# Kernel tuning notes

Measured on AMD Instinct MI355X. Metric: run time of the kernel, lower is better.

Reference implementation:

```python
import jax, jax.numpy as jnp
import numpy as np

H, W = 32, 56
CK, CV = 64, 512
N = 16 * H * W  # long + work memory fully populated: 16 frames of H*W entries
TOP_K = 30


def setup_inputs() -> dict:
    key = jax.random.key(0)
    k1, k2, k3, k4, k5 = jax.random.split(key, 5)
    return {
        "q_key": jax.random.normal(k1, (1, CK, H, W), dtype=jnp.float32),
        "q_selection": jax.random.uniform(k2, (1, CK, H, W), dtype=jnp.float32),
        "mem_key": jax.random.normal(k3, (1, CK, N), dtype=jnp.float32),
        "mem_shrinkage": jax.random.uniform(k4, (1, N, 1), dtype=jnp.float32),
        "mem_value": jax.random.normal(k5, (2, CV, N), dtype=jnp.float32),
    }


def reference(q_key, q_selection, mem_key, mem_shrinkage, mem_value):
    b, ck, h, w = q_key.shape
    hw = h * w
    qk = q_key.reshape(1, ck, hw)          # [1, CK, HW]
    qs = q_selection.reshape(1, ck, hw)    # [1, CK, HW]

    mk = jnp.swapaxes(mem_key, 1, 2)       # [1, N, CK]
    # negative weighted squared L2 distance via matmul algebra
    a_sq = jnp.matmul(mk * mk, qs)                    # [1, N, HW]
    two_ab = 2.0 * jnp.matmul(mk, qk * qs)            # [1, N, HW]
    b_sq = jnp.sum(qs * qk * qk, axis=1, keepdims=True)  # [1, 1, HW]
    sim = (-a_sq + two_ab - b_sq) * mem_shrinkage / jnp.sqrt(jnp.float32(ck))  # [1, N, HW]

    # topk over the memory axis (dim=1), softmax over selected entries, scatter back
    simT = jnp.swapaxes(sim, 1, 2)                    # [1, HW, N]
    vals, idx = jax.lax.top_k(simT, TOP_K)            # [1, HW, K]
    x_exp = jnp.exp(vals)
    x_exp = x_exp / jnp.sum(x_exp, axis=-1, keepdims=True)
    i0 = jnp.arange(1)[:, None, None]
    i1 = jnp.arange(hw)[None, :, None]
    affT = jnp.zeros_like(simT).at[i0, i1, idx].set(x_exp)  # [1, HW, N]
    affinity = jnp.swapaxes(affT, 1, 2)               # [1, N, HW]

    out = jnp.matmul(mem_value, affinity)             # [2, CV, HW] (batch-broadcast)
    return out.reshape(2, CV, h, w)
```

## Files before the change

### kernel.cpp

```cpp
#include <hip/hip_runtime.h>
#include <math.h>

#define HW      1792
#define NMEM    28672
#define NCHUNK  3584
#define TOPK    30
#define KSEL    48
#define SCAP    64
#define SIMB    448
#define WPS     7

typedef __attribute__((ext_vector_type(8))) short bf16x8;
typedef __attribute__((ext_vector_type(8))) unsigned short u16x8;
typedef __attribute__((ext_vector_type(4))) float f32x4;
typedef __attribute__((ext_vector_type(4))) _Float16 h4;
typedef unsigned long long ull;

static __device__ __forceinline__ unsigned short f2bf(float v) {
  unsigned b = __float_as_uint(v);
  return (unsigned short)((b + 0x7FFFu + ((b >> 16) & 1u)) >> 16);
}
static __device__ __forceinline__ float bf2f(unsigned short h) {
  return __uint_as_float(((unsigned)h) << 16);
}
static __device__ __forceinline__ unsigned fkey(float v) {
  return __float_as_uint(-v) & 0x7FFFFFFFu;
}
static __device__ __forceinline__ ull umax64(ull a, ull b) { return a > b ? a : b; }
static __device__ __forceinline__ ull umin64(ull a, ull b) { return a < b ? a : b; }
static __device__ __forceinline__ void gl_lds16(const void* g, void* l) {
  __builtin_amdgcn_global_load_lds(
      (const __attribute__((address_space(1))) unsigned*)g,
      (__attribute__((address_space(3))) unsigned*)l, 16, 0, 0);
}
#define WSYNC() do { asm volatile("s_waitcnt lgkmcnt(0)" ::: "memory"); \
                     __builtin_amdgcn_wave_barrier(); } while (0)

__global__ __launch_bounds__(256)
void k_prep_b(const float* __restrict__ mk, const float* __restrict__ shr_in,
              unsigned short* __restrict__ Bh,
              float* __restrict__ mkT, float* __restrict__ shr_s)
{
  const int n = blockIdx.x * 256 + threadIdx.x;
  shr_s[n] = shr_in[n] * 0.125f;
  for (int cb = 0; cb < 64; cb += 8) {
    u16x8 h1, h2;
    float vv[8];
    #pragma unroll
    for (int j = 0; j < 8; ++j) {
      float v = mk[(size_t)(cb + j) * NMEM + n];
      vv[j] = v;
      h1[j] = f2bf(v);
      h2[j] = f2bf(v * v);
    }
    const int s = cb >> 3;
    *reinterpret_cast<u16x8*>(&Bh[((size_t)s * NMEM + n) * 8])       = h1;
    *reinterpret_cast<u16x8*>(&Bh[((size_t)(s + 8) * NMEM + n) * 8]) = h2;
    *reinterpret_cast<float4*>(&mkT[(size_t)n * 64 + cb])     = make_float4(vv[0], vv[1], vv[2], vv[3]);
    *reinterpret_cast<float4*>(&mkT[(size_t)n * 64 + cb + 4]) = make_float4(vv[4], vv[5], vv[6], vv[7]);
  }
}

__global__ __launch_bounds__(256)
void k_prep_u(const float* __restrict__ q_key, const float* __restrict__ q_sel,
              unsigned short* __restrict__ Uh, unsigned short* __restrict__ Ul,
              float* __restrict__ bsq)
{
  const int p = blockIdx.x * 256 + threadIdx.x;
  float bs = 0.f;
  for (int cb = 0; cb < 64; cb += 8) {
    u16x8 h1, l1, h2, l2;
    #pragma unroll
    for (int j = 0; j < 8; ++j) {
      int c = cb + j;
      float k = q_key[(size_t)c * HW + p];
      float s = q_sel[(size_t)c * HW + p];
      float u = 2.f * k * s;
      float w = -s;
      bs = fmaf(s * k, k, bs);
      unsigned short h = f2bf(u); h1[j] = h; l1[j] = f2bf(u - bf2f(h));
      unsigned short g = f2bf(w); h2[j] = g; l2[j] = f2bf(w - bf2f(g));
    }
    const int s = cb >> 3;
    *reinterpret_cast<u16x8*>(&Uh[((size_t)s * HW + p) * 8])       = h1;
    *reinterpret_cast<u16x8*>(&Ul[((size_t)s * HW + p) * 8])       = l1;
    *reinterpret_cast<u16x8*>(&Uh[((size_t)(s + 8) * HW + p) * 8]) = h2;
    *reinterpret_cast<u16x8*>(&Ul[((size_t)(s + 8) * HW + p) * 8]) = l2;
  }
  bsq[p] = bs;
}

__global__ __launch_bounds__(256, 2)
void k_sim(const unsigned short* __restrict__ Uh, const unsigned short* __restrict__ Ul,
           const unsigned short* __restrict__ Bh,
           const float* __restrict__ bsq, const float* __restrict__ shr_s,
           float* __restrict__ pmax)
{
  __shared__ char smem[65536] __attribute__((aligned(16)));
  const int tid = threadIdx.x;
  const int wid = tid >> 6, lane = tid & 63;
  const int lr = lane & 15, lg = lane >> 4;
  const int pb = blockIdx.x % 14, st = blockIdx.x / 14;
  const int pw = pb * 128 + wid * 32;
  const int w0 = st * WPS;

  bf16x8 a0h[4], a0l[4], a1h[4], a1l[4];
  #pragma unroll
  for (int t = 0; t < 4; ++t) {
    const size_t e0 = ((size_t)(t * 4 + lg) * HW + pw + lr) * 8;
    const size_t e1 = e0 + 16 * 8;
    a0h[t] = *reinterpret_cast<const bf16x8*>(&Uh[e0]);
    a0l[t] = *reinterpret_cast<const bf16x8*>(&Ul[e0]);
    a1h[t] = *reinterpret_cast<const bf16x8*>(&Uh[e1]);
    a1l[t] = *reinterpret_cast<const bf16x8*>(&Ul[e1]);
  }
  float bq[2][4];
  #pragma unroll
  for (int pt = 0; pt < 2; ++pt)
    #pragma unroll
    for (int r = 0; r < 4; ++r) bq[pt][r] = bsq[pw + pt * 16 + 4 * lg + r];

  auto stage = [&](int buf, int i) {
    const int n0 = (w0 + i) * 128;
    #pragma unroll
    for (int j = 0; j < 8; ++j) {
      const int idx = j * 256 + tid;
      const int s = idx >> 7, rr = idx & 127;
      gl_lds16((const char*)Bh + ((size_t)s * NMEM + n0 + rr) * 16,
               smem + buf * 32768 + idx * 16);
    }
  };

  stage(0, 0);
  int buf = 0;
  for (int i = 0; i < WPS; ++i) {
    __syncthreads();
    if (i + 1 < WPS) stage(buf ^ 1, i + 1);

    f32x4 acc[2][8];
    #pragma unroll
    for (int a = 0; a < 2; ++a)
      #pragma unroll
      for (int b = 0; b < 8; ++b) acc[a][b] = (f32x4){0.f, 0.f, 0.f, 0.f};

    const short* lb = (const short*)(smem + buf * 32768);
    #pragma unroll
    for (int t = 0; t < 4; ++t) {
      #pragma unroll
      for (int nt = 0; nt < 8; ++nt) {
        bf16x8 bh = *reinterpret_cast<const bf16x8*>(
            &lb[((t * 4 + lg) * 128 + nt * 16 + lr) * 8]);
        acc[0][nt] = __builtin_amdgcn_mfma_f32_16x16x32_bf16(a0h[t], bh, acc[0][nt], 0, 0, 0);
        acc[0][nt] = __builtin_amdgcn_mfma_f32_16x16x32_bf16(a0l[t], bh, acc[0][nt], 0, 0, 0);
        acc[1][nt] = __builtin_amdgcn_mfma_f32_16x16x32_bf16(a1h[t], bh, acc[1][nt], 0, 0, 0);
        acc[1][nt] = __builtin_amdgcn_mfma_f32_16x16x32_bf16(a1l[t], bh, acc[1][nt], 0, 0, 0);
      }
    }

    const int wgl = w0 + i;
    const int n0 = wgl * 128;
    float shv[8];
    #pragma unroll
    for (int nt = 0; nt < 8; ++nt) shv[nt] = shr_s[n0 + nt * 16 + lr];
    #pragma unroll
    for (int pt = 0; pt < 2; ++pt) {
      #pragma unroll
      for (int r = 0; r < 4; ++r) {
        float mx = -INFINITY;
        #pragma unroll
        for (int nt = 0; nt < 8; ++nt)
          mx = fmaxf(mx, (acc[pt][nt][r] - bq[pt][r]) * shv[nt]);
        pmax[(size_t)(pw + pt * 16 + 4 * lg + r) * NCHUNK + wgl * 16 + lr] = mx;
      }
    }
    buf ^= 1;
  }
}

__global__ __launch_bounds__(256, 2)
void k_select(const float* __restrict__ pmax, const float* __restrict__ mkT,
              const float* __restrict__ q_key, const float* __restrict__ q_sel,
              const float* __restrict__ shr_s,
              float* __restrict__ wgt, int* __restrict__ widx)
{
  __shared__ ull   cand[4][512];
  __shared__ ull   fin[4][256];
  __shared__ short sl[4][SCAP];
  __shared__ float sqk[4][64], sqs[4][64];

  const int w = threadIdx.x >> 6, lane = threadIdx.x & 63;
  const int pix = blockIdx.x * 4 + w;
  ull*   cd = cand[w];
  ull*   fn = fin[w];
  short* sv = sl[w];

  sqk[w][lane] = q_key[(size_t)lane * HW + pix];
  sqs[w][lane] = q_sel[(size_t)lane * HW + pix];

  unsigned kk[56];
  const float* pm = pmax + (size_t)pix * NCHUNK;
  #pragma unroll
  for (int j = 0; j < 56; ++j) kk[j] = fkey(pm[lane + 64 * j]);

  unsigned lo = 0, hi = 0x7FFFFFFFu;
  while (lo < hi) {
    unsigned mid = (lo + hi) >> 1;
    int c = 0;
    #pragma unroll
    for (int j = 0; j < 56; ++j) c += (kk[j] <= mid);
    #pragma unroll
    for (int off = 1; off < 64; off <<= 1) c += __shfl_xor(c, off);
    if (c >= KSEL) hi = mid; else lo = mid + 1;
  }
  const unsigned T48 = lo;

  int ns = 0;
  #pragma unroll
  for (int j = 0; j < 56; ++j) {
    bool keep = (kk[j] <= T48);
    ull ball = __ballot(keep);
    if (keep) {
      int pos = ns + __popcll(ball & ((1ull << lane) - 1ull));
      if (pos < SCAP) sv[pos] = (short)(lane + 64 * j);
    }
    ns += __popcll(ball);
  }
  ns = (ns < SCAP) ? ns : SCAP;
  const int NC = ns * 8;
  WSYNC();

  const float4* k4p = reinterpret_cast<const float4*>(sqk[w]);
  const float4* s4p = reinterpret_cast<const float4*>(sqs[w]);
  ull myp[8];
  #pragma unroll
  for (int i = 0; i < 8; ++i) {
    myp[i] = 0ull;
    const int c = lane + (i << 6);
    if (c < NC) {
      const int cc = sv[c >> 3];
      const int n = ((cc >> 4) << 7) + (cc & 15) + ((c & 7) << 4);
      const float4* mr = reinterpret_cast<const float4*>(mkT + (size_t)n * 64);
      float s0 = 0.f, s1 = 0.f, s2 = 0.f, s3 = 0.f;
      #pragma unroll
      for (int j = 0; j < 4; ++j) {
        float4 q0 = mr[4*j], q1 = mr[4*j+1], q2 = mr[4*j+2], q3 = mr[4*j+3];
        float4 a0 = k4p[4*j], a1 = k4p[4*j+1], a2 = k4p[4*j+2], a3 = k4p[4*j+3];
        float4 b0 = s4p[4*j], b1 = s4p[4*j+1], b2 = s4p[4*j+2], b3 = s4p[4*j+3];
        float d;
        d = q0.x-a0.x; s0 = fmaf(b0.x*d, d, s0);
        d = q0.y-a0.y; s1 = fmaf(b0.y*d, d, s1);
        d = q0.z-a0.z; s2 = fmaf(b0.z*d, d, s2);
        d = q0.w-a0.w; s3 = fmaf(b0.w*d, d, s3);
        d = q1.x-a1.x; s0 = fmaf(b1.x*d, d, s0);
        d = q1.y-a1.y; s1 = fmaf(b1.y*d, d, s1);
        d = q1.z-a1.z; s2 = fmaf(b1.z*d, d, s2);
        d = q1.w-a1.w; s3 = fmaf(b1.w*d, d, s3);
        d = q2.x-a2.x; s0 = fmaf(b2.x*d, d, s0);
        d = q2.y-a2.y; s1 = fmaf(b2.y*d, d, s1);
        d = q2.z-a2.z; s2 = fmaf(b2.z*d, d, s2);
        d = q2.w-a2.w; s3 = fmaf(b2.w*d, d, s3);
        d = q3.x-a3.x; s0 = fmaf(b3.x*d, d, s0);
        d = q3.y-a3.y; s1 = fmaf(b3.y*d, d, s1);
        d = q3.z-a3.z; s2 = fmaf(b3.z*d, d, s2);
        d = q3.w-a3.w; s3 = fmaf(b3.w*d, d, s3);
      }
      float svv = -((s0 + s1) + (s2 + s3)) * shr_s[n];
      myp[i] = ((ull)(0x7FFFFFFFu - fkey(svv)) << 32) |
               (ull)(0xFFFFFFFFu - (unsigned)n);
    }
    cd[lane + (i << 6)] = myp[i];
  }
  WSYNC();

  ull p0 = 0, p1 = 0, p2 = 0, p3 = 0;
  #pragma unroll
  for (int i = 0; i < 8; ++i) {
    ull k = myp[i], m;
    m = umax64(p0, k); k = umin64(p0, k); p0 = m;
    m = umax64(p1, k); k = umin64(p1, k); p1 = m;
    m = umax64(p2, k); k = umin64(p2, k); p2 = m;
    m = umax64(p3, k); k = umin64(p3, k); p3 = m;
  }
  fn[lane * 4 + 0] = p0; fn[lane * 4 + 1] = p1;
  fn[lane * 4 + 2] = p2; fn[lane * 4 + 3] = p3;
  WSYNC();

  int r0 = 0, r1 = 0, r2 = 0, r3 = 0;
  for (int k = 0; k < 256; ++k) {
    ull kb = fn[k];
    r0 += (kb > p0); r1 += (kb > p1); r2 += (kb > p2); r3 += (kb > p3);
  }
  ull c30 = (r0 == TOPK - 1) ? p0 : (r1 == TOPK - 1) ? p1 :
            (r2 == TOPK - 1) ? p2 : (r3 == TOPK - 1) ? p3 : 0ull;
  ull ball2 = __ballot(c30 != 0ull);
  ull k30 = __shfl(c30, (int)(__ffsll((long long)ball2) - 1));

  int cnt = 0;
  #pragma unroll
  for (int i = 0; i < 8; ++i) cnt += (myp[i] > k30);
  #pragma unroll
  for (int off = 32; off > 0; off >>= 1) cnt += __shfl_xor(cnt, off);
  const bool ok = (cnt == TOPK - 1);

  if (ok) {
    float v0 = -__uint_as_float(0x7FFFFFFFu - (unsigned)(p0 >> 32));
    float v1 = -__uint_as_float(0x7FFFFFFFu - (unsigned)(p1 >> 32));
    float v2 = -__uint_as_float(0x7FFFFFFFu - (unsigned)(p2 >> 32));
    float v3 = -__uint_as_float(0x7FFFFFFFu - (unsigned)(p3 >> 32));
    float e0 = (r0 < TOPK) ? expf(v0) : 0.f;
    float e1 = (r1 < TOPK) ? expf(v1) : 0.f;
    float e2 = (r2 < TOPK) ? expf(v2) : 0.f;
    float e3 = (r3 < TOPK) ? expf(v3) : 0.f;
    float es = e0 + e1 + e2 + e3;
    #pragma unroll
    for (int off = 32; off > 0; off >>= 1) es += __shfl_xor(es, off);
    if (r0 < TOPK) { wgt[(size_t)pix*32 + r0] = e0/es; widx[(size_t)pix*32 + r0] = (int)(0xFFFFFFFFu - (unsigned)(p0 & 0xFFFFFFFFu)); }
    if (r1 < TOPK) { wgt[(size_t)pix*32 + r1] = e1/es; widx[(size_t)pix*32 + r1] = (int)(0xFFFFFFFFu - (unsigned)(p1 & 0xFFFFFFFFu)); }
    if (r2 < TOPK) { wgt[(size_t)pix*32 + r2] = e2/es; widx[(size_t)pix*32 + r2] = (int)(0xFFFFFFFFu - (unsigned)(p2 & 0xFFFFFFFFu)); }
    if (r3 < TOPK) { wgt[(size_t)pix*32 + r3] = e3/es; widx[(size_t)pix*32 + r3] = (int)(0xFFFFFFFFu - (unsigned)(p3 & 0xFFFFFFFFu)); }
  } else {
    int rr[8];
    #pragma unroll
    for (int i = 0; i < 8; ++i) rr[i] = 0;
    for (int k = 0; k < NC; ++k) {
      ull kb = cd[k];
      #pragma unroll
      for (int i = 0; i < 8; ++i) rr[i] += (kb > myp[i]);
    }
    float ev[8]; float es = 0.f;
    #pragma unroll
    for (int i = 0; i < 8; ++i) {
      float vv = -__uint_as_float(0x7FFFFFFFu - (unsigned)(myp[i] >> 32));
      ev[i] = (myp[i] != 0ull && rr[i] < TOPK) ? expf(vv) : 0.f;
      es += ev[i];
    }
    #pragma unroll
    for (int off = 32; off > 0; off >>= 1) es += __shfl_xor(es, off);
    #pragma unroll
    for (int i = 0; i < 8; ++i) {
      if (myp[i] != 0ull && rr[i] < TOPK) {
        wgt [(size_t)pix * 32 + rr[i]] = ev[i] / es;
        widx[(size_t)pix * 32 + rr[i]] = (int)(0xFFFFFFFFu - (unsigned)(myp[i] & 0xFFFFFFFFu));
      }
    }
  }
}

__global__ __launch_bounds__(256)
void k_transpose_h(const float* __restrict__ mv, _Float16* __restrict__ mvT)
{
  __shared__ float t[64][65];
  const int n0 = blockIdx.x * 64, ch0 = blockIdx.y * 64;
  const int tid = threadIdx.x;
  for (int i = tid; i < 64 * 16; i += 256) {
    int r = i >> 4, c4 = (i & 15) << 2;
    float4 v = *reinterpret_cast<const float4*>(&mv[(size_t)(ch0 + r) * NMEM + n0 + c4]);
    t[r][c4] = v.x; t[r][c4 + 1] = v.y; t[r][c4 + 2] = v.z; t[r][c4 + 3] = v.w;
  }
  __syncthreads();
  for (int i = tid; i < 64 * 16; i += 256) {
    int r = i >> 4, c4 = (i & 15) << 2;
    h4 hv = {(_Float16)t[c4][r], (_Float16)t[c4 + 1][r],
             (_Float16)t[c4 + 2][r], (_Float16)t[c4 + 3][r]};
    *reinterpret_cast<h4*>(&mvT[(size_t)(n0 + r) * 1024 + ch0 + c4]) = hv;
  }
}

__global__ __launch_bounds__(256)
void k_gather_h(const _Float16* __restrict__ mvT, const float* __restrict__ wgt,
                const int* __restrict__ widx, float* __restrict__ out)
{
  __shared__ float sw[8][TOPK];
  __shared__ int   si[8][TOPK];
  __shared__ float sbuf[256][9];
  const int p0 = blockIdx.x * 8, chg = blockIdx.y * 256;
  const int tid = threadIdx.x;

  for (int i = tid; i < 8 * TOPK; i += 256) {
    int q = i / TOPK, k = i - q * TOPK;
    sw[q][k] = wgt [(size_t)(p0 + q) * 32 + k];
    si[q][k] = widx[(size_t)(p0 + q) * 32 + k];
  }
  __syncthreads();

  const int ch = chg + tid;
  #pragma unroll 2
  for (int q = 0; q < 8; ++q) {
    float a = 0.f;
    #pragma unroll
    for (int k = 0; k < TOPK; ++k)
      a = fmaf(sw[q][k], (float)mvT[(size_t)si[q][k] * 1024 + ch], a);
    sbuf[tid][q] = a;
  }
  __syncthreads();

  for (int i = tid; i < 256 * 8; i += 256) {
    int cl = i >> 3, q = i & 7;
    out[(size_t)(chg + cl) * HW + p0 + q] = sbuf[cl][q];
  }
}

__global__ __launch_bounds__(256)
void k_gather_f(const float* __restrict__ src, const float* __restrict__ wgt,
                const int* __restrict__ widx, float* __restrict__ out,
                long n_stride, long ch_stride)
{
  __shared__ float sw[8][TOPK];
  __shared__ int   si[8][TOPK];
  __shared__ float sbuf[256][9];
  const int p0 = blockIdx.x * 8, chg = blockIdx.y * 256;
  const int tid = threadIdx.x;

  for (int i = tid; i < 8 * TOPK; i += 256) {
    int q = i / TOPK, k = i - q * TOPK;
    sw[q][k] = wgt [(size_t)(p0 + q) * 32 + k];
    si[q][k] = widx[(size_t)(p0 + q) * 32 + k];
  }
  __syncthreads();

  const int ch = chg + tid;
  #pragma unroll 2
  for (int q = 0; q < 8; ++q) {
    float a = 0.f;
    #pragma unroll
    for (int k = 0; k < TOPK; ++k)
      a = fmaf(sw[q][k], src[(size_t)si[q][k] * n_stride + (size_t)ch * ch_stride], a);
    sbuf[tid][q] = a;
  }
  __syncthreads();

  for (int i = tid; i < 256 * 8; i += 256) {
    int cl = i >> 3, q = i & 7;
    out[(size_t)(chg + cl) * HW + p0 + q] = sbuf[cl][q];
  }
}

extern "C" void kernel_launch(void* const* d_in, const int* in_sizes, int n_in,
                              void* d_out, int out_size, void* d_ws, size_t ws_size,
                              hipStream_t stream)
{
  (void)in_sizes; (void)n_in; (void)out_size;
  const float* q_key     = (const float*)d_in[0];
  const float* q_sel     = (const float*)d_in[1];
  const float* mem_key   = (const float*)d_in[2];
  const float* mem_shr   = (const float*)d_in[3];
  const float* mem_value = (const float*)d_in[4];
  float* out = (float*)d_out;

  char* ws = (char*)d_ws;
  size_t off = 0;
  auto alloc = [&](size_t b) { size_t c = off; off = (off + b + 255) & ~(size_t)255; return c; };
  size_t o_w   = alloc((size_t)HW * 32 * 4);
  size_t o_wi  = alloc((size_t)HW * 32 * 4);
  size_t o_pr  = off;
  size_t o_bh  = alloc((size_t)NMEM * 128 * 2);
  size_t o_uh  = alloc((size_t)HW * 128 * 2);
  size_t o_ul  = alloc((size_t)HW * 128 * 2);
  size_t o_bsq = alloc((size_t)HW * 4);
  size_t o_shr = alloc((size_t)NMEM * 4);
  size_t o_mkT = alloc((size_t)NMEM * 64 * 4);
  size_t o_pm  = alloc((size_t)HW * NCHUNK * 4);
  size_t o_end = off;

  float*          wg   = (float*)(ws + o_w);
  int*            wi   = (int*)  (ws + o_wi);
  unsigned short* Bh   = (unsigned short*)(ws + o_bh);
  unsigned short* Uh   = (unsigned short*)(ws + o_uh);
  unsigned short* Ul   = (unsigned short*)(ws + o_ul);
  float*          bsq  = (float*)(ws + o_bsq);
  float*          shr  = (float*)(ws + o_shr);
  float*          mkT  = (float*)(ws + o_mkT);
  float*          pmx  = (float*)(ws + o_pm);

  const size_t mvh_sz = (size_t)NMEM * 1024 * 2;

  k_prep_b<<<NMEM / 256, 256, 0, stream>>>(mem_key, mem_shr, Bh, mkT, shr);
  k_prep_u<<<HW / 256, 256, 0, stream>>>(q_key, q_sel, Uh, Ul, bsq);
  k_sim<<<SIMB, 256, 0, stream>>>(Uh, Ul, Bh, bsq, shr, pmx);

  if (ws_size >= o_end + mvh_sz) {
    _Float16* mvT = (_Float16*)(ws + o_end);
    k_transpose_h<<<dim3(NMEM / 64, 16), 256, 0, stream>>>(mem_value, mvT);
    k_select<<<HW / 4, 256, 0, stream>>>(pmx, mkT, q_key, q_sel, shr, wg, wi);
    k_gather_h<<<dim3(HW / 8, 4), 256, 0, stream>>>(mvT, wg, wi, out);
  } else if (ws_size >= o_pr + mvh_sz) {
    k_select<<<HW / 4, 256, 0, stream>>>(pmx, mkT, q_key, q_sel, shr, wg, wi);
    _Float16* mvT = (_Float16*)(ws + o_pr);
    k_transpose_h<<<dim3(NMEM / 64, 16), 256, 0, stream>>>(mem_value, mvT);
    k_gather_h<<<dim3(HW / 8, 4), 256, 0, stream>>>(mvT, wg, wi, out);
  } else {
    k_select<<<HW / 4, 256, 0, stream>>>(pmx, mkT, q_key, q_sel, shr, wg, wi);
    k_gather_f<<<dim3(HW / 8, 4), 256, 0, stream>>>(
        mem_value, wg, wi, out, 1, NMEM);
  }
}
```

Before: 150.2 us.

## Fuse mem_value transpose blocks into the select kernel launch

Merges the fp16 transpose of mem_value into the top-k select kernel as a single launch. Blocks are interleaved so that one in every 17 does pixel selection and the rest transpose 64x64 tiles, with the shared memory of both roles overlaid through a union. This removes one kernel launch and lets the memory-bound transpose run alongside the latency-bound select work. The cost is a larger shared-memory footprint per block for the transpose blocks, plus some branch overhead.

```diff
diff --git a/kernel.cpp b/kernel.cpp
--- a/kernel.cpp
+++ b/kernel.cpp
@@ -9,6 +9,7 @@
 #define SCAP    64
 #define SIMB    448
 #define WPS     7
+#define NSELB   448
 
 typedef __attribute__((ext_vector_type(8))) short bf16x8;
 typedef __attribute__((ext_vector_type(8))) unsigned short u16x8;
@@ -177,25 +178,58 @@
   }
 }
 
+struct SelS {
+  ull   cand[4][512];
+  ull   fin[4][256];
+  short sl[4][SCAP];
+  float sqk[4][64], sqs[4][64];
+};
+union SMemU { SelS sel; float tt[64][65]; };
+
 __global__ __launch_bounds__(256, 2)
-void k_select(const float* __restrict__ pmax, const float* __restrict__ mkT,
-              const float* __restrict__ q_key, const float* __restrict__ q_sel,
-              const float* __restrict__ shr_s,
-              float* __restrict__ wgt, int* __restrict__ widx)
-{
-  __shared__ ull   cand[4][512];
-  __shared__ ull   fin[4][256];
-  __shared__ short sl[4][SCAP];
-  __shared__ float sqk[4][64], sqs[4][64];
-
-  const int w = threadIdx.x >> 6, lane = threadIdx.x & 63;
-  const int pix = blockIdx.x * 4 + w;
-  ull*   cd = cand[w];
-  ull*   fn = fin[w];
-  short* sv = sl[w];
-
-  sqk[w][lane] = q_key[(size_t)lane * HW + pix];
-  sqs[w][lane] = q_sel[(size_t)lane * HW + pix];
+void k_selT(const float* __restrict__ pmax, const float* __restrict__ mkT,
+            const float* __restrict__ q_key, const float* __restrict__ q_sel,
+            const float* __restrict__ shr_s,
+            float* __restrict__ wgt, int* __restrict__ widx,
+            const float* __restrict__ mv, _Float16* __restrict__ mvT)
+{
+  __shared__ SMemU sm;
+  const int tid = threadIdx.x;
+
+  int sg = -1, tb = -1;
+  if (gridDim.x > NSELB) {
+    const int g = blockIdx.x / 17, r = blockIdx.x % 17;
+    if (r == 0) sg = g; else tb = g * 16 + (r - 1);
+  } else {
+    sg = blockIdx.x;
+  }
+
+  if (tb >= 0) {
+    const int n0 = (tb % 448) * 64, ch0 = (tb / 448) * 64;
+    for (int i = tid; i < 64 * 16; i += 256) {
+      int r = i >> 4, c4 = (i & 15) << 2;
+      float4 v = *reinterpret_cast<const float4*>(&mv[(size_t)(ch0 + r) * NMEM + n0 + c4]);
+      sm.tt[r][c4] = v.x; sm.tt[r][c4 + 1] = v.y;
+      sm.tt[r][c4 + 2] = v.z; sm.tt[r][c4 + 3] = v.w;
+    }
+    __syncthreads();
+    for (int i = tid; i < 64 * 16; i += 256) {
+      int r = i >> 4, c4 = (i & 15) << 2;
+      h4 hv = {(_Float16)sm.tt[c4][r], (_Float16)sm.tt[c4 + 1][r],
+               (_Float16)sm.tt[c4 + 2][r], (_Float16)sm.tt[c4 + 3][r]};
+      *reinterpret_cast<h4*>(&mvT[(size_t)(n0 + r) * 1024 + ch0 + c4]) = hv;
+    }
+    return;
+  }
+
+  const int w = tid >> 6, lane = tid & 63;
+  const int pix = sg * 4 + w;
+  ull*   cd = sm.sel.cand[w];
+  ull*   fn = sm.sel.fin[w];
+  short* sv = sm.sel.sl[w];
+
+  sm.sel.sqk[w][lane] = q_key[(size_t)lane * HW + pix];
+  sm.sel.sqs[w][lane] = q_sel[(size_t)lane * HW + pix];
 
   unsigned kk[56];
   const float* pm = pmax + (size_t)pix * NCHUNK;
@@ -229,8 +263,8 @@
   const int NC = ns * 8;
   WSYNC();
 
-  const float4* k4p = reinterpret_cast<const float4*>(sqk[w]);
-  const float4* s4p = reinterpret_cast<const float4*>(sqs[w]);
+  const float4* k4p = reinterpret_cast<const float4*>(sm.sel.sqk[w]);
+  const float4* s4p = reinterpret_cast<const float4*>(sm.sel.sqs[w]);
   ull myp[8];
   #pragma unroll
   for (int i = 0; i < 8; ++i) {
@@ -480,16 +514,18 @@
 
   if (ws_size >= o_end + mvh_sz) {
     _Float16* mvT = (_Float16*)(ws + o_end);
-    k_transpose_h<<<dim3(NMEM / 64, 16), 256, 0, stream>>>(mem_value, mvT);
-    k_select<<<HW / 4, 256, 0, stream>>>(pmx, mkT, q_key, q_sel, shr, wg, wi);
+    k_selT<<<NSELB * 17, 256, 0, stream>>>(pmx, mkT, q_key, q_sel, shr,
+                                           wg, wi, mem_value, mvT);
     k_gather_h<<<dim3(HW / 8, 4), 256, 0, stream>>>(mvT, wg, wi, out);
   } else if (ws_size >= o_pr + mvh_sz) {
-    k_select<<<HW / 4, 256, 0, stream>>>(pmx, mkT, q_key, q_sel, shr, wg, wi);
+    k_selT<<<NSELB, 256, 0, stream>>>(pmx, mkT, q_key, q_sel, shr,
+                                      wg, wi, mem_value, nullptr);
     _Float16* mvT = (_Float16*)(ws + o_pr);
     k_transpose_h<<<dim3(NMEM / 64, 16), 256, 0, stream>>>(mem_value, mvT);
     k_gather_h<<<dim3(HW / 8, 4), 256, 0, stream>>>(mvT, wg, wi, out);
   } else {
-    k_select<<<HW / 4, 256, 0, stream>>>(pmx, mkT, q_key, q_sel, shr, wg, wi);
+    k_selT<<<NSELB, 256, 0, stream>>>(pmx, mkT, q_key, q_sel, shr,
+                                      wg, wi, mem_value, nullptr);
     k_gather_f<<<dim3(HW / 8, 4), 256, 0, stream>>>(
         mem_value, wg, wi, out, 1, NMEM);
   }
```

Measured after the change: 155.4 us. +3.5%, slower.
